# Kernel optimization log

Hardware: AMD Instinct MI355X
Metric: run time of the kernel (lower is better)

Reference implementation:

```python
import jax, jax.numpy as jnp
import numpy as np

IOU_THRESH = 0.6
NEG = -1.0  # strictly below any real IoU (IoU >= 0), used to mask cross-label pairs


def cxcywh_to_xyxy(b):
    cx, cy, w, h = b[..., 0], b[..., 1], b[..., 2], b[..., 3]
    return jnp.stack([cx - 0.5 * w, cy - 0.5 * h, cx + 0.5 * w, cy + 0.5 * h], axis=-1)


def pairwise_iou(a, b):
    # a: [M,4] xyxy, b: [N,4] xyxy -> [M,N]
    area_a = (a[:, 2] - a[:, 0]) * (a[:, 3] - a[:, 1])
    area_b = (b[:, 2] - b[:, 0]) * (b[:, 3] - b[:, 1])
    lt = jnp.maximum(a[:, None, :2], b[None, :, :2])
    rb = jnp.minimum(a[:, None, 2:], b[None, :, 2:])
    wh = jnp.clip(rb - lt, 0.0, None)
    inter = wh[..., 0] * wh[..., 1]
    union = area_a[:, None] + area_b[None, :] - inter
    return inter / jnp.maximum(union, 1e-9)


def assign_one(proposals, prompt_inds, gt_boxes, gt_labels, k):
    # Vectorized equivalent of the per-unique-label loop: masking IoU to NEG for
    # cross-label (gt, proposal) pairs reproduces the per-group matcher exactly.
    M = gt_boxes.shape[0]
    match = gt_labels[:, None] == prompt_inds[None, :]                # [M,N] group membership
    iou = pairwise_iou(cxcywh_to_xyxy(gt_boxes), cxcywh_to_xyxy(proposals))  # [M,N]
    miou = jnp.where(match, iou, NEG)                                 # group-masked IoU
    best_iou = miou.max(axis=0)                                       # [N] matcher argmax within group
    best_gt = miou.argmax(axis=0)
    valid_prop = match.any(axis=0)                                    # proposal's label appears in gt
    gmax = miou.max(axis=1)                                           # [M] per-gt best IoU in its group
    lq = (miou == gmax[:, None]) & match                              # allow_low_quality_matches
    pos = valid_prop & ((best_iou >= IOU_THRESH) | lq.any(axis=0))    # matched_labels == 1 (foreground)
    # positives assigned to each gt (fg cap num_queries*0.25 never binds at these sizes)
    counts = jax.ops.segment_sum(pos.astype(jnp.int32), best_gt, num_segments=M)
    # sample_topk_per_gt: per gt take top min(count, k) proposals by group IoU
    topv, topi = jax.lax.top_k(miou, k)                               # [M,k]
    take = jnp.minimum(counts, k)
    valid = jnp.arange(k)[None, :] < take[:, None]                    # [M,k]
    rows = jnp.where(valid, topi, -1)                                 # proposal indices, -1 padded
    cols = jnp.where(valid, jnp.arange(M)[:, None], -1)               # gt indices, -1 padded
    sel_iou = jnp.where(valid, topv, 0.0)
    return rows, cols, valid, sel_iou


def setup_inputs() -> dict:
    key = jax.random.key(0)
    ks = jax.random.split(key, 6)
    B, N, M, L = 16, 3000, 300, 80

    def boxes(k, shape):
        u = jax.random.uniform(k, shape + (4,), dtype=jnp.float32)
        cxcy = u[..., :2]
        wh = 0.02 + 0.28 * u[..., 2:]  # cxcywh with positive extents
        return jnp.concatenate([cxcy, wh], axis=-1)

    return {
        "pred_logits_match": jax.random.normal(ks[0], (B, N, 1), dtype=jnp.float32),
        "pred_boxes": boxes(ks[1], (B, N)),
        "init_reference": boxes(ks[2], (B, N)),
        "prompt_inds": jax.random.randint(ks[3], (B, N), 0, L, dtype=jnp.int32),
        "gt_labels": jax.random.randint(ks[4], (B, M), 0, L, dtype=jnp.int32),
        "gt_boxes": boxes(ks[5], (B, M)),
        "max_k": 4,
    }


def reference(pred_logits_match, pred_boxes, init_reference, prompt_inds, gt_labels, gt_boxes, max_k):
    _ = jax.nn.sigmoid(pred_logits_match)  # computed in the original forward but unused downstream
    f = lambda p, pi, gb, gl: assign_one(p, pi, gb, gl, max_k)
    rows, cols, valid, sel_iou = jax.vmap(f)(init_reference, prompt_inds, gt_boxes, gt_labels)
    # padded equivalent of the list of (rows, cols) index pairs; valid marks real entries
    return rows, cols, valid, sel_iou
```

## Files before the change

### kernel.cpp

```cpp
#include <hip/hip_runtime.h>

#define BB 16
#define NN 3000
#define MM 300
#define LL 80
#define KK 4
#define IOU_THRESH 0.6f

typedef unsigned long long u64;

struct Box { float x1, y1, x2, y2, area; };

__device__ __forceinline__ Box to_xyxy(float4 b) {
#pragma clang fp contract(off)
    Box r;
    r.x1 = b.x - 0.5f * b.z;
    r.y1 = b.y - 0.5f * b.w;
    r.x2 = b.x + 0.5f * b.z;
    r.y2 = b.y + 0.5f * b.w;
    r.area = (r.x2 - r.x1) * (r.y2 - r.y1);
    return r;
}

__device__ __forceinline__ float pair_iou(Box a, Box b) {
#pragma clang fp contract(off)
    float ltx = fmaxf(a.x1, b.x1);
    float lty = fmaxf(a.y1, b.y1);
    float rbx = fminf(a.x2, b.x2);
    float rby = fminf(a.y2, b.y2);
    float wx = fmaxf(rbx - ltx, 0.0f);
    float wy = fmaxf(rby - lty, 0.0f);
    float inter = wx * wy;
    float uni = a.area + b.area - inter;
    return inter / fmaxf(uni, 1e-9f);
}

__device__ __forceinline__ unsigned int f32_to_ordered(float f) {
    unsigned int u = __float_as_uint(f);
    return (u & 0x80000000u) ? ~u : (u | 0x80000000u);
}
__device__ __forceinline__ float ordered_to_f32(unsigned int u) {
    unsigned int b = (u & 0x80000000u) ? (u & 0x7FFFFFFFu) : ~u;
    return __uint_as_float(b);
}

__device__ __forceinline__ u64 umax64(u64 a, u64 b) { return a > b ? a : b; }
__device__ __forceinline__ u64 umin64(u64 a, u64 b) { return a < b ? a : b; }

__device__ __forceinline__ u64 shfl_xor_u64(u64 v, int mask) {
    int lo = __shfl_xor((int)(unsigned)v, mask, 64);
    int hi = __shfl_xor((int)(unsigned)(v >> 32), mask, 64);
    return ((u64)(unsigned)hi << 32) | (u64)(unsigned)lo;
}

__device__ __forceinline__ void topins(u64 t[4], u64 k) {
    u64 c0 = umin64(t[0], k);
    t[0] = umax64(t[0], k);
    u64 c1 = umin64(t[1], c0);
    t[1] = umax64(t[1], c0);
    u64 c2 = umin64(t[2], c1);
    t[2] = umax64(t[2], c1);
    t[3] = umax64(t[3], c2);
}

__device__ __forceinline__ void wave_merge_top4(u64 t[4]) {
    #pragma unroll
    for (int s = 1; s < 64; s <<= 1) {
        u64 b0 = shfl_xor_u64(t[0], s);
        u64 b1 = shfl_xor_u64(t[1], s);
        u64 b2 = shfl_xor_u64(t[2], s);
        u64 b3 = shfl_xor_u64(t[3], s);
        u64 a0 = t[0], a1 = t[1], a2 = t[2], a3 = t[3];
        t[0] = umax64(a0, b0);
        t[1] = umax64(umin64(a0, b0), umax64(a1, b1));
        t[2] = umax64(umax64(a2, b2), umax64(umin64(a0, b1), umin64(a1, b0)));
        t[3] = umax64(umax64(a3, b3),
               umax64(umin64(a0, b2), umax64(umin64(a1, b1), umin64(a2, b0))));
    }
}

__global__ __launch_bounds__(256) void kBin(const int* __restrict__ pinds,
                                            const int* __restrict__ glab,
                                            unsigned short* __restrict__ pidx,
                                            int* __restrict__ pstart,
                                            int* __restrict__ pcnt,
                                            unsigned short* __restrict__ gidx,
                                            int* __restrict__ gstart,
                                            int* __restrict__ gcnt,
                                            int* __restrict__ counts) {
    int b = blockIdx.x;
    int tid = threadIdx.x;
    __shared__ int hist[LL], cur[LL], gh[LL], gcur[LL];
    if (tid < LL) { hist[tid] = 0; gh[tid] = 0; }
    __syncthreads();
    for (int n = tid; n < NN; n += 256) atomicAdd(&hist[pinds[b * NN + n]], 1);
    for (int m = tid; m < MM; m += 256) atomicAdd(&gh[glab[b * MM + m]], 1);
    __syncthreads();
    if (tid < LL) {
        int s = 0;
        for (int j = 0; j < tid; ++j) s += hist[j];
        cur[tid] = s; pstart[b * LL + tid] = s; pcnt[b * LL + tid] = hist[tid];
        int t = 0;
        for (int j = 0; j < tid; ++j) t += gh[j];
        gcur[tid] = t; gstart[b * LL + tid] = t; gcnt[b * LL + tid] = gh[tid];
    }
    __syncthreads();
    for (int n = tid; n < NN; n += 256) {
        int l = pinds[b * NN + n];
        int pos = atomicAdd(&cur[l], 1);
        pidx[b * NN + pos] = (unsigned short)n;
    }
    for (int m = tid; m < MM; m += 256) {
        int l = glab[b * MM + m];
        int pos = atomicAdd(&gcur[l], 1);
        gidx[b * MM + pos] = (unsigned short)m;
    }
    for (int i = tid; i < MM; i += 256) counts[b * MM + i] = 0;
}

__global__ __launch_bounds__(256) void kTop(const float4* __restrict__ props,
                                            const int*    __restrict__ glab,
                                            const float4* __restrict__ gbox,
                                            const unsigned short* __restrict__ pidx,
                                            const int* __restrict__ pstart,
                                            const int* __restrict__ pcnt,
                                            const unsigned short* __restrict__ gidx,
                                            float* out) {
    int b = blockIdx.y;
    int wv = __builtin_amdgcn_readfirstlane((int)(threadIdx.x >> 6));
    int lane = threadIdx.x & 63;
    int g = blockIdx.x * 4 + wv;
    int m = gidx[b * MM + g];
    int bm = b * MM + m;
    Box gt = to_xyxy(gbox[bm]);
    int l = glab[bm];
    int s = pstart[b * LL + l], c = pcnt[b * LL + l];

    const u64 init = ((u64)f32_to_ordered(-1.0f) << 32);
    u64 t[4] = {init, init, init, init};
    for (int i = lane; i < c; i += 64) {
        int n = pidx[b * NN + s + i];
        Box pb = to_xyxy(props[(size_t)b * NN + n]);
        float iou = pair_iou(gt, pb);
        u64 key = ((u64)f32_to_ordered(iou) << 32) |
                  (u64)(0xFFFFFFFFu - (unsigned)n);
        topins(t, key);
    }
    wave_merge_top4(t);

    if (lane == 0) {
        float gm = ordered_to_f32((unsigned)(t[0] >> 32));
        float* topv = out + 2 * KK * BB * MM / KK * KK;
        int*   topi = (int*)(out + 3 * BB * MM * KK / 1);
        topv = out + 2 * BB * MM * KK / 2;
        topv = out + 38400;
        topi = (int*)(out + 57600);
        #pragma unroll
        for (int j = 0; j < KK; ++j) {
            topv[bm * KK + j] = ordered_to_f32((unsigned)(t[j] >> 32));
            topi[bm * KK + j] = (int)(0xFFFFFFFFu - (unsigned)t[j]);
        }
        float4* gtb = (float4*)out;
        int gpos = b * MM + g;
        gtb[gpos * 2 + 0] = make_float4(gt.x1, gt.y1, gt.x2, gt.y2);
        gtb[gpos * 2 + 1] = make_float4(gt.area, gm, __int_as_float(m), 0.0f);
    }
}

__global__ __launch_bounds__(256) void kAsn(const float4* __restrict__ props,
                                            const int*    __restrict__ pinds,
                                            const int* __restrict__ gstart,
                                            const int* __restrict__ gcnt,
                                            const float* __restrict__ out,
                                            int* __restrict__ counts) {
    int b = blockIdx.y;
    int n = blockIdx.x * 256 + threadIdx.x;
    if (n >= NN) return;
    float4 pr = props[(size_t)b * NN + n];
    int lbl = pinds[(size_t)b * NN + n];
    Box pb = to_xyxy(pr);
    int s = gstart[b * LL + lbl], c = gcnt[b * LL + lbl];
    const float4* gtb = (const float4*)out;

    u64 key = 0;
    bool lq = false;
    for (int j = 0; j < c; ++j) {
        int idx = (b * MM + s + j) * 2;
        float4 q0 = gtb[idx], q1 = gtb[idx + 1];
        Box a; a.x1 = q0.x; a.y1 = q0.y; a.x2 = q0.z; a.y2 = q0.w; a.area = q1.x;
        float iou = pair_iou(a, pb);
        int m = __float_as_int(q1.z);
        u64 k = ((u64)f32_to_ordered(iou) << 32) |
                (u64)(0xFFFFFFFFu - (unsigned)m);
        key = umax64(key, k);
        lq = lq || (iou == q1.y);
    }
    if (c > 0) {
        float v = ordered_to_f32((unsigned)(key >> 32));
        int bm = (int)(0xFFFFFFFFu - (unsigned)key);
        if ((v >= IOU_THRESH) || lq) atomicAdd(&counts[b * MM + bm], 1);
    }
}

__global__ __launch_bounds__(256) void kC(const int* __restrict__ counts,
                                          float* out) {
    int i = blockIdx.x * 256 + threadIdx.x;
    if (i >= BB * MM) return;
    int m = i % MM;
    int take = min(counts[i], KK);
    float4 tv = ((const float4*)(out + 38400))[i];
    int4   ti = ((const int4*)(out + 57600))[i];
    float4 rows, cols, valid, sel;
    rows.x = (0 < take) ? (float)ti.x : -1.0f;
    rows.y = (1 < take) ? (float)ti.y : -1.0f;
    rows.z = (2 < take) ? (float)ti.z : -1.0f;
    rows.w = (3 < take) ? (float)ti.w : -1.0f;
    cols.x = (0 < take) ? (float)m : -1.0f;
    cols.y = (1 < take) ? (float)m : -1.0f;
    cols.z = (2 < take) ? (float)m : -1.0f;
    cols.w = (3 < take) ? (float)m : -1.0f;
    valid.x = (0 < take) ? 1.0f : 0.0f;
    valid.y = (1 < take) ? 1.0f : 0.0f;
    valid.z = (2 < take) ? 1.0f : 0.0f;
    valid.w = (3 < take) ? 1.0f : 0.0f;
    sel.x = (0 < take) ? tv.x : 0.0f;
    sel.y = (1 < take) ? tv.y : 0.0f;
    sel.z = (2 < take) ? tv.z : 0.0f;
    sel.w = (3 < take) ? tv.w : 0.0f;
    float4* o = (float4*)out;
    const int CH4 = BB * MM;
    o[0 * CH4 + i] = rows;
    o[1 * CH4 + i] = cols;
    o[2 * CH4 + i] = valid;
    o[3 * CH4 + i] = sel;
}

extern "C" void kernel_launch(void* const* d_in, const int* in_sizes, int n_in,
                              void* d_out, int out_size, void* d_ws, size_t ws_size,
                              hipStream_t stream) {
    const float4* props = (const float4*)d_in[2];
    const int*    pinds = (const int*)d_in[3];
    const int*    glab  = (const int*)d_in[4];
    const float4* gbox  = (const float4*)d_in[5];
    float* out = (float*)d_out;

    char* w = (char*)d_ws;
    int*   counts = (int*)w;                 w += BB * MM * sizeof(int);
    int*   pstart = (int*)w;                 w += BB * LL * sizeof(int);
    int*   pcnt   = (int*)w;                 w += BB * LL * sizeof(int);
    int*   gstart = (int*)w;                 w += BB * LL * sizeof(int);
    int*   gcnt   = (int*)w;                 w += BB * LL * sizeof(int);
    unsigned short* pidx = (unsigned short*)w; w += BB * NN * sizeof(short);
    unsigned short* gidx = (unsigned short*)w;

    kBin<<<BB, 256, 0, stream>>>(pinds, glab, pidx, pstart, pcnt,
                                 gidx, gstart, gcnt, counts);
    dim3 gT(MM / 4, BB);
    kTop<<<gT, 256, 0, stream>>>(props, glab, gbox, pidx, pstart, pcnt, gidx, out);
    dim3 gA((NN + 255) / 256, BB);
    kAsn<<<gA, 256, 0, stream>>>(props, pinds, gstart, gcnt, out, counts);
    kC<<<(BB * MM + 255) / 256, 256, 0, stream>>>(counts, out);
}
```

Measured before the change: 90.15 us.

## Fuse assignment and output kernels into one per-batch block with shared-memory counts

```diff
diff --git a/kernel.cpp b/kernel.cpp
--- a/kernel.cpp
+++ b/kernel.cpp
@@ -86,8 +86,7 @@
                                             int* __restrict__ pcnt,
                                             unsigned short* __restrict__ gidx,
                                             int* __restrict__ gstart,
-                                            int* __restrict__ gcnt,
-                                            int* __restrict__ counts) {
+                                            int* __restrict__ gcnt) {
     int b = blockIdx.x;
     int tid = threadIdx.x;
     __shared__ int hist[LL], cur[LL], gh[LL], gcur[LL];
@@ -115,7 +114,6 @@
         int pos = atomicAdd(&gcur[l], 1);
         gidx[b * MM + pos] = (unsigned short)m;
     }
-    for (int i = tid; i < MM; i += 256) counts[b * MM + i] = 0;
 }
 
 __global__ __launch_bounds__(256) void kTop(const float4* __restrict__ props,
@@ -125,7 +123,9 @@
                                             const int* __restrict__ pstart,
                                             const int* __restrict__ pcnt,
                                             const unsigned short* __restrict__ gidx,
-                                            float* out) {
+                                            float*  __restrict__ topv,
+                                            int*    __restrict__ topi,
+                                            float4* __restrict__ grec) {
     int b = blockIdx.y;
     int wv = __builtin_amdgcn_readfirstlane((int)(threadIdx.x >> 6));
     int lane = threadIdx.x & 63;
@@ -150,89 +150,97 @@
 
     if (lane == 0) {
         float gm = ordered_to_f32((unsigned)(t[0] >> 32));
-        float* topv = out + 2 * KK * BB * MM / KK * KK;
-        int*   topi = (int*)(out + 3 * BB * MM * KK / 1);
-        topv = out + 2 * BB * MM * KK / 2;
-        topv = out + 38400;
-        topi = (int*)(out + 57600);
         #pragma unroll
         for (int j = 0; j < KK; ++j) {
             topv[bm * KK + j] = ordered_to_f32((unsigned)(t[j] >> 32));
             topi[bm * KK + j] = (int)(0xFFFFFFFFu - (unsigned)t[j]);
         }
-        float4* gtb = (float4*)out;
         int gpos = b * MM + g;
-        gtb[gpos * 2 + 0] = make_float4(gt.x1, gt.y1, gt.x2, gt.y2);
-        gtb[gpos * 2 + 1] = make_float4(gt.area, gm, __int_as_float(m), 0.0f);
-    }
-}
-
-__global__ __launch_bounds__(256) void kAsn(const float4* __restrict__ props,
+        grec[gpos * 2 + 0] = make_float4(gt.x1, gt.y1, gt.x2, gt.y2);
+        grec[gpos * 2 + 1] = make_float4(gt.area, gm, __int_as_float(m), 0.0f);
+    }
+}
+
+__global__ __launch_bounds__(256) void kFin(const float4* __restrict__ props,
                                             const int*    __restrict__ pinds,
-                                            const int* __restrict__ gstart,
-                                            const int* __restrict__ gcnt,
-                                            const float* __restrict__ out,
-                                            int* __restrict__ counts) {
-    int b = blockIdx.y;
-    int n = blockIdx.x * 256 + threadIdx.x;
-    if (n >= NN) return;
-    float4 pr = props[(size_t)b * NN + n];
-    int lbl = pinds[(size_t)b * NN + n];
-    Box pb = to_xyxy(pr);
-    int s = gstart[b * LL + lbl], c = gcnt[b * LL + lbl];
-    const float4* gtb = (const float4*)out;
-
-    u64 key = 0;
-    bool lq = false;
-    for (int j = 0; j < c; ++j) {
-        int idx = (b * MM + s + j) * 2;
-        float4 q0 = gtb[idx], q1 = gtb[idx + 1];
-        Box a; a.x1 = q0.x; a.y1 = q0.y; a.x2 = q0.z; a.y2 = q0.w; a.area = q1.x;
-        float iou = pair_iou(a, pb);
-        int m = __float_as_int(q1.z);
-        u64 k = ((u64)f32_to_ordered(iou) << 32) |
-                (u64)(0xFFFFFFFFu - (unsigned)m);
-        key = umax64(key, k);
-        lq = lq || (iou == q1.y);
-    }
-    if (c > 0) {
-        float v = ordered_to_f32((unsigned)(key >> 32));
-        int bm = (int)(0xFFFFFFFFu - (unsigned)key);
-        if ((v >= IOU_THRESH) || lq) atomicAdd(&counts[b * MM + bm], 1);
-    }
-}
-
-__global__ __launch_bounds__(256) void kC(const int* __restrict__ counts,
-                                          float* out) {
-    int i = blockIdx.x * 256 + threadIdx.x;
-    if (i >= BB * MM) return;
-    int m = i % MM;
-    int take = min(counts[i], KK);
-    float4 tv = ((const float4*)(out + 38400))[i];
-    int4   ti = ((const int4*)(out + 57600))[i];
-    float4 rows, cols, valid, sel;
-    rows.x = (0 < take) ? (float)ti.x : -1.0f;
-    rows.y = (1 < take) ? (float)ti.y : -1.0f;
-    rows.z = (2 < take) ? (float)ti.z : -1.0f;
-    rows.w = (3 < take) ? (float)ti.w : -1.0f;
-    cols.x = (0 < take) ? (float)m : -1.0f;
-    cols.y = (1 < take) ? (float)m : -1.0f;
-    cols.z = (2 < take) ? (float)m : -1.0f;
-    cols.w = (3 < take) ? (float)m : -1.0f;
-    valid.x = (0 < take) ? 1.0f : 0.0f;
-    valid.y = (1 < take) ? 1.0f : 0.0f;
-    valid.z = (2 < take) ? 1.0f : 0.0f;
-    valid.w = (3 < take) ? 1.0f : 0.0f;
-    sel.x = (0 < take) ? tv.x : 0.0f;
-    sel.y = (1 < take) ? tv.y : 0.0f;
-    sel.z = (2 < take) ? tv.z : 0.0f;
-    sel.w = (3 < take) ? tv.w : 0.0f;
-    float4* o = (float4*)out;
-    const int CH4 = BB * MM;
-    o[0 * CH4 + i] = rows;
-    o[1 * CH4 + i] = cols;
-    o[2 * CH4 + i] = valid;
-    o[3 * CH4 + i] = sel;
+                                            const float*  __restrict__ topv,
+                                            const int*    __restrict__ topi,
+                                            const float4* __restrict__ grec,
+                                            const int*    __restrict__ gstart,
+                                            const int*    __restrict__ gcnt,
+                                            float* __restrict__ out) {
+    int b = blockIdx.x;
+    int tid = threadIdx.x;
+
+    __shared__ float4 sg[MM * 2];
+    __shared__ int scnt[MM];
+    __shared__ int gst[LL], gcn[LL];
+
+    for (int i = tid; i < MM * 2; i += 256) sg[i] = grec[b * MM * 2 + i];
+    for (int i = tid; i < MM; i += 256) scnt[i] = 0;
+    if (tid < LL) {
+        gst[tid] = gstart[b * LL + tid];
+        gcn[tid] = gcnt[b * LL + tid];
+    }
+    __syncthreads();
+
+    for (int n = tid; n < NN; n += 256) {
+        Box pb = to_xyxy(props[(size_t)b * NN + n]);
+        int l = pinds[b * NN + n];
+        int s = gst[l];
+        int c = gcn[l];
+        u64 key = 0;
+        bool lq = false;
+        for (int j = 0; j < c; ++j) {
+            float4 q0 = sg[(s + j) * 2];
+            float4 q1 = sg[(s + j) * 2 + 1];
+            Box a;
+            a.x1 = q0.x; a.y1 = q0.y; a.x2 = q0.z; a.y2 = q0.w;
+            a.area = q1.x;
+            float iou = pair_iou(a, pb);
+            int m = __float_as_int(q1.z);
+            u64 k = ((u64)f32_to_ordered(iou) << 32) |
+                    (u64)(0xFFFFFFFFu - (unsigned)m);
+            key = umax64(key, k);
+            lq = lq || (iou == q1.y);
+        }
+        if (c > 0) {
+            float v = ordered_to_f32((unsigned)(key >> 32));
+            int bm = (int)(0xFFFFFFFFu - (unsigned)key);
+            if ((v >= IOU_THRESH) || lq) atomicAdd(&scnt[bm], 1);
+        }
+    }
+    __syncthreads();
+
+    for (int m = tid; m < MM; m += 256) {
+        int i = b * MM + m;
+        int take = min(scnt[m], KK);
+        float4 tv = ((const float4*)topv)[i];
+        int4   ti = ((const int4*)topi)[i];
+        float4 rows, cols, valid, sel;
+        rows.x = (0 < take) ? (float)ti.x : -1.0f;
+        rows.y = (1 < take) ? (float)ti.y : -1.0f;
+        rows.z = (2 < take) ? (float)ti.z : -1.0f;
+        rows.w = (3 < take) ? (float)ti.w : -1.0f;
+        cols.x = (0 < take) ? (float)m : -1.0f;
+        cols.y = (1 < take) ? (float)m : -1.0f;
+        cols.z = (2 < take) ? (float)m : -1.0f;
+        cols.w = (3 < take) ? (float)m : -1.0f;
+        valid.x = (0 < take) ? 1.0f : 0.0f;
+        valid.y = (1 < take) ? 1.0f : 0.0f;
+        valid.z = (2 < take) ? 1.0f : 0.0f;
+        valid.w = (3 < take) ? 1.0f : 0.0f;
+        sel.x = (0 < take) ? tv.x : 0.0f;
+        sel.y = (1 < take) ? tv.y : 0.0f;
+        sel.z = (2 < take) ? tv.z : 0.0f;
+        sel.w = (3 < take) ? tv.w : 0.0f;
+        float4* o = (float4*)out;
+        const int CH4 = BB * MM;
+        o[0 * CH4 + i] = rows;
+        o[1 * CH4 + i] = cols;
+        o[2 * CH4 + i] = valid;
+        o[3 * CH4 + i] = sel;
+    }
 }
 
 extern "C" void kernel_launch(void* const* d_in, const int* in_sizes, int n_in,
@@ -245,19 +253,21 @@
     float* out = (float*)d_out;
 
     char* w = (char*)d_ws;
-    int*   counts = (int*)w;                 w += BB * MM * sizeof(int);
-    int*   pstart = (int*)w;                 w += BB * LL * sizeof(int);
-    int*   pcnt   = (int*)w;                 w += BB * LL * sizeof(int);
-    int*   gstart = (int*)w;                 w += BB * LL * sizeof(int);
-    int*   gcnt   = (int*)w;                 w += BB * LL * sizeof(int);
-    unsigned short* pidx = (unsigned short*)w; w += BB * NN * sizeof(short);
+    float*  topv   = (float*)w;  w += (size_t)BB * MM * KK * sizeof(float);
+    int*    topi   = (int*)w;    w += (size_t)BB * MM * KK * sizeof(int);
+    float4* grec   = (float4*)w; w += (size_t)BB * MM * 2 * sizeof(float4);
+    int*    pstart = (int*)w;    w += (size_t)BB * LL * sizeof(int);
+    int*    pcnt   = (int*)w;    w += (size_t)BB * LL * sizeof(int);
+    int*    gstart = (int*)w;    w += (size_t)BB * LL * sizeof(int);
+    int*    gcnt   = (int*)w;    w += (size_t)BB * LL * sizeof(int);
+    unsigned short* pidx = (unsigned short*)w; w += (size_t)BB * NN * 2;
     unsigned short* gidx = (unsigned short*)w;
 
     kBin<<<BB, 256, 0, stream>>>(pinds, glab, pidx, pstart, pcnt,
-                                 gidx, gstart, gcnt, counts);
+                                 gidx, gstart, gcnt);
     dim3 gT(MM / 4, BB);
-    kTop<<<gT, 256, 0, stream>>>(props, glab, gbox, pidx, pstart, pcnt, gidx, out);
-    dim3 gA((NN + 255) / 256, BB);
-    kAsn<<<gA, 256, 0, stream>>>(props, pinds, gstart, gcnt, out, counts);
-    kC<<<(BB * MM + 255) / 256, 256, 0, stream>>>(counts, out);
-}
+    kTop<<<gT, 256, 0, stream>>>(props, glab, gbox, pidx, pstart, pcnt, gidx,
+                                 topv, topi, grec);
+    kFin<<<BB, 256, 0, stream>>>(props, pinds, topv, topi, grec,
+                                 gstart, gcnt, out);
+}
```

Result: slower. 106.3 us (+17.9%).
